# Performance work log

Measured on AMD Instinct MI355X. Metric: run time of the kernel, lower is better.

The kernel has to match this reference:

```python
import jax, jax.numpy as jnp
import numpy as np

ED = 1024
NH = 16
HD = ED // NH


def setup_inputs() -> dict:
    key = jax.random.key(0)
    ks = jax.random.split(key, 9)
    s = 1.0 / np.sqrt(ED)
    return {
        "x": jax.random.normal(ks[0], (2, 2048, ED), dtype=jnp.float32),
        "wq": jax.random.uniform(ks[1], (ED, ED), jnp.float32, -s, s),
        "bq": jax.random.uniform(ks[2], (ED,), jnp.float32, -s, s),
        "wk": jax.random.uniform(ks[3], (ED, ED), jnp.float32, -s, s),
        "bk": jax.random.uniform(ks[4], (ED,), jnp.float32, -s, s),
        "wv": jax.random.uniform(ks[5], (ED, ED), jnp.float32, -s, s),
        "bv": jax.random.uniform(ks[6], (ED,), jnp.float32, -s, s),
        "wo": jax.random.uniform(ks[7], (ED, ED), jnp.float32, -s, s),
        "bo": jax.random.uniform(ks[8], (ED,), jnp.float32, -s, s),
    }


def reference(x, wq, bq, wk, bk, wv, bv, wo, bo):
    B, N, _ = x.shape
    # projections; weights stored as [out, in] like nn.Linear -> x @ W.T + b
    def proj(w, b):
        y = jnp.einsum('bnd,ed->bne', x, w) + b
        return y.reshape(B, N, NH, HD).transpose(0, 2, 1, 3)  # [B, H, N, hd]
    Q, K, V = proj(wq, bq), proj(wk, bk), proj(wv, bv)
    scores = jnp.einsum('bhnd,bhmd->bhnm', Q, K) / jnp.sqrt(jnp.float32(HD))
    attn = jax.nn.softmax(scores, axis=-1)
    ctx = jnp.einsum('bhnm,bhmd->bhnd', attn, V)
    ctx = ctx.transpose(0, 2, 1, 3).reshape(B, N, ED)
    return jnp.einsum('bne,de->bnd', ctx, wo) + bo
```

## Files before the change

kernel.cpp:

```cpp
#include <hip/hip_runtime.h>
#include <hip/hip_bf16.h>

#define ED 1024
#define NH 16
#define HD 64
#define SEQ 2048

typedef float f32x4 __attribute__((ext_vector_type(4)));
typedef float f32x16 __attribute__((ext_vector_type(16)));
typedef short s16x8 __attribute__((ext_vector_type(8)));
typedef short s16x4 __attribute__((ext_vector_type(4)));
typedef __attribute__((address_space(1))) const unsigned int GBuf;
typedef __attribute__((address_space(3))) unsigned int LBuf;

#define QSC 0.18033688011112042f

union BF8 { s16x8 v; __hip_bfloat16 h[8]; };

__device__ __forceinline__ unsigned cvt_pk_bf16(float lo, float hi) {
  unsigned r;
  asm("v_cvt_pk_bf16_f32 %0, %1, %2" : "=v"(r) : "v"(lo), "v"(hi));
  return r;
}

__device__ __forceinline__ s16x8 pack_pfrag(float p0, float p1, float p2, float p3,
                                            float p4, float p5, float p6, float p7) {
  unsigned w0 = cvt_pk_bf16(p0, p1), w1 = cvt_pk_bf16(p2, p3);
  unsigned w2 = cvt_pk_bf16(p4, p5), w3 = cvt_pk_bf16(p6, p7);
  asm("v_permlane32_swap_b32 %0, %1" : "+v"(w0), "+v"(w2));
  asm("v_permlane32_swap_b32 %0, %1" : "+v"(w1), "+v"(w3));
  union { unsigned u[4]; s16x8 v; } r;
  r.u[0] = w0; r.u[1] = w1; r.u[2] = w2; r.u[3] = w3;
  return r.v;
}

__device__ inline void cvt_one(const float* __restrict__ s, __hip_bfloat16* __restrict__ d,
                               int n, int t, int stride) {
  const int n8 = n >> 3;
  for (int i = t; i < n8; i += stride) {
    const float4 u = ((const float4*)s)[2 * i];
    const float4 v = ((const float4*)s)[2 * i + 1];
    BF8 o;
    o.h[0] = __float2bfloat16(u.x); o.h[1] = __float2bfloat16(u.y);
    o.h[2] = __float2bfloat16(u.z); o.h[3] = __float2bfloat16(u.w);
    o.h[4] = __float2bfloat16(v.x); o.h[5] = __float2bfloat16(v.y);
    o.h[6] = __float2bfloat16(v.z); o.h[7] = __float2bfloat16(v.w);
    ((s16x8*)d)[i] = o.v;
  }
}

__global__ __launch_bounds__(256) void cvt5(const float* s0, const float* s1, const float* s2,
                                            const float* s3, const float* s4,
                                            __hip_bfloat16* d0, __hip_bfloat16* d1,
                                            __hip_bfloat16* d2, __hip_bfloat16* d3,
                                            __hip_bfloat16* d4,
                                            int n0, int n1, int n2, int n3, int n4) {
  const int stride = gridDim.x * blockDim.x;
  const int t = blockIdx.x * blockDim.x + threadIdx.x;
  cvt_one(s0, d0, n0, t, stride);
  cvt_one(s1, d1, n1, t, stride);
  cvt_one(s2, d2, n2, t, stride);
  cvt_one(s3, d3, n3, t, stride);
  cvt_one(s4, d4, n4, t, stride);
}

__global__ __launch_bounds__(256) void gemm_qkv(const __hip_bfloat16* __restrict__ A,
                                                const __hip_bfloat16* __restrict__ wq,
                                                const float* __restrict__ bq,
                                                const __hip_bfloat16* __restrict__ wk,
                                                const float* __restrict__ bk,
                                                const __hip_bfloat16* __restrict__ wv,
                                                const float* __restrict__ bv,
                                                __hip_bfloat16* __restrict__ Qo,
                                                __hip_bfloat16* __restrict__ Ko,
                                                __hip_bfloat16* __restrict__ Vo) {
  __shared__ __hip_bfloat16 As[2][128 * 64];
  __shared__ __hip_bfloat16 Bs[2][128 * 64];

  const int lin = (blockIdx.z * 32 + blockIdx.y) * 8 + blockIdx.x;
  const int work = (lin & 7) * 96 + (lin >> 3);
  const int z = work >> 8;
  const int rem = work & 255;
  const int m0 = (rem >> 3) * 128, n0 = (rem & 7) * 128;

  const __hip_bfloat16* W = (z == 0) ? wq : (z == 1) ? wk : wv;
  const float* bias = (z == 0) ? bq : (z == 1) ? bk : bv;

  const int tid = threadIdx.x;
  const int wave = tid >> 6, lane = tid & 63;
  const int ln15 = lane & 15, lg = lane >> 4;
  const int wr = (wave >> 1) * 64, wc = (wave & 1) * 64;

  f32x4 acc[4][4];
#pragma unroll
  for (int i = 0; i < 4; i++)
#pragma unroll
    for (int j = 0; j < 4; j++) acc[i][j] = (f32x4){0.f, 0.f, 0.f, 0.f};

  const int srow = tid >> 3;
  const int sk = (tid & 7) * 8;

  auto STAGE = [&](int t, int buf) {
    const int k0 = t * 64;
#pragma unroll
    for (int c = 0; c < 4; c++) {
      const int r = c * 32 + srow;
      __builtin_amdgcn_global_load_lds((GBuf*)(A + (size_t)(m0 + r) * ED + k0 + sk),
                                       (LBuf*)((char*)&As[buf][0] + c * 4096 + tid * 16), 16, 0, 0);
      __builtin_amdgcn_global_load_lds((GBuf*)(W + (size_t)(n0 + r) * ED + k0 + sk),
                                       (LBuf*)((char*)&Bs[buf][0] + c * 4096 + tid * 16), 16, 0, 0);
    }
  };

  const int NT = ED / 64;
  STAGE(0, 0);
  __syncthreads();
  for (int t = 0; t < NT; t++) {
    const int cur = t & 1;
    if (t + 1 < NT) STAGE(t + 1, cur ^ 1);
    __builtin_amdgcn_s_setprio(1);
#pragma unroll
    for (int kb = 0; kb < 2; kb++) {
      const int kof = kb * 32 + lg * 8;
      s16x8 a[4], b[4];
#pragma unroll
      for (int i = 0; i < 4; i++)
        a[i] = *(const s16x8*)&As[cur][(wr + i * 16 + ln15) * 64 + kof];
#pragma unroll
      for (int j = 0; j < 4; j++)
        b[j] = *(const s16x8*)&Bs[cur][(wc + j * 16 + ln15) * 64 + kof];
#pragma unroll
      for (int i = 0; i < 4; i++)
#pragma unroll
        for (int j = 0; j < 4; j++)
          acc[i][j] = __builtin_amdgcn_mfma_f32_16x16x32_bf16(a[i], b[j], acc[i][j], 0, 0, 0);
    }
    __builtin_amdgcn_s_setprio(0);
    __syncthreads();
  }

  const float scale = (z == 0) ? QSC : 1.0f;
  if (z < 2) {
    __hip_bfloat16* out = (z == 0) ? Qo : Ko;
#pragma unroll
    for (int j = 0; j < 4; j++) {
      const int e = n0 + wc + j * 16 + ln15;
      const float bvv = bias[e];
      const int h = e >> 6, hd = e & 63;
#pragma unroll
      for (int i = 0; i < 4; i++) {
#pragma unroll
        for (int r = 0; r < 4; r++) {
          const int m = m0 + wr + i * 16 + lg * 4 + r;
          const int b = m >> 11, n = m & 2047;
          out[(((size_t)(b * NH + h)) * SEQ + n) * HD + hd] =
              __float2bfloat16((acc[i][j][r] + bvv) * scale);
        }
      }
    }
  } else {
#pragma unroll
    for (int j = 0; j < 4; j++) {
      const int e = n0 + wc + j * 16 + ln15;
      const float bvv = bias[e];
      const int h = e >> 6, hd = e & 63;
#pragma unroll
      for (int i = 0; i < 4; i++) {
        const int m = m0 + wr + i * 16 + lg * 4;
        const int b = m >> 11, n = m & 2047;
        union { s16x4 v; __hip_bfloat16 hh[4]; } pk;
#pragma unroll
        for (int r = 0; r < 4; r++) pk.hh[r] = __float2bfloat16(acc[i][j][r] + bvv);
        *(s16x4*)&Vo[(((size_t)(b * NH + h)) * HD + hd) * SEQ + n] = pk.v;
      }
    }
  }
}

__global__ __launch_bounds__(256) void gemm_out(const __hip_bfloat16* __restrict__ A,
                                                const __hip_bfloat16* __restrict__ W,
                                                const float* __restrict__ bias,
                                                float* __restrict__ out) {
  __shared__ __hip_bfloat16 As[2][128 * 64];
  __shared__ __hip_bfloat16 Bs[2][128 * 64];

  const int lin = blockIdx.y * 8 + blockIdx.x;
  const int work = (lin & 7) * 32 + (lin >> 3);
  const int m0 = (work >> 3) * 128, n0 = (work & 7) * 128;

  const int tid = threadIdx.x;
  const int wave = tid >> 6, lane = tid & 63;
  const int ln15 = lane & 15, lg = lane >> 4;
  const int wr = (wave >> 1) * 64, wc = (wave & 1) * 64;

  f32x4 acc[4][4];
#pragma unroll
  for (int i = 0; i < 4; i++)
#pragma unroll
    for (int j = 0; j < 4; j++) acc[i][j] = (f32x4){0.f, 0.f, 0.f, 0.f};

  const int srow = tid >> 3;
  const int sk = (tid & 7) * 8;

  auto STAGE = [&](int t, int buf) {
    const int k0 = t * 64;
#pragma unroll
    for (int c = 0; c < 4; c++) {
      const int r = c * 32 + srow;
      __builtin_amdgcn_global_load_lds((GBuf*)(A + (size_t)(m0 + r) * ED + k0 + sk),
                                       (LBuf*)((char*)&As[buf][0] + c * 4096 + tid * 16), 16, 0, 0);
      __builtin_amdgcn_global_load_lds((GBuf*)(W + (size_t)(n0 + r) * ED + k0 + sk),
                                       (LBuf*)((char*)&Bs[buf][0] + c * 4096 + tid * 16), 16, 0, 0);
    }
  };

  const int NT = ED / 64;
  STAGE(0, 0);
  __syncthreads();
  for (int t = 0; t < NT; t++) {
    const int cur = t & 1;
    if (t + 1 < NT) STAGE(t + 1, cur ^ 1);
    __builtin_amdgcn_s_setprio(1);
#pragma unroll
    for (int kb = 0; kb < 2; kb++) {
      const int kof = kb * 32 + lg * 8;
      s16x8 a[4], b[4];
#pragma unroll
      for (int i = 0; i < 4; i++)
        a[i] = *(const s16x8*)&As[cur][(wr + i * 16 + ln15) * 64 + kof];
#pragma unroll
      for (int j = 0; j < 4; j++)
        b[j] = *(const s16x8*)&Bs[cur][(wc + j * 16 + ln15) * 64 + kof];
#pragma unroll
      for (int i = 0; i < 4; i++)
#pragma unroll
        for (int j = 0; j < 4; j++)
          acc[i][j] = __builtin_amdgcn_mfma_f32_16x16x32_bf16(a[i], b[j], acc[i][j], 0, 0, 0);
    }
    __builtin_amdgcn_s_setprio(0);
    __syncthreads();
  }

#pragma unroll
  for (int j = 0; j < 4; j++) {
    const int e = n0 + wc + j * 16 + ln15;
    const float bvv = bias[e];
#pragma unroll
    for (int i = 0; i < 4; i++)
#pragma unroll
      for (int r = 0; r < 4; r++) {
        const int m = m0 + wr + i * 16 + lg * 4 + r;
        out[(size_t)m * ED + e] = acc[i][j][r] + bvv;
      }
  }
}

__global__ __launch_bounds__(256) void attn_bf16(const __hip_bfloat16* __restrict__ Q,
                                                 const __hip_bfloat16* __restrict__ K,
                                                 const __hip_bfloat16* __restrict__ VT,
                                                 __hip_bfloat16* __restrict__ CTX) {
  __shared__ __hip_bfloat16 KsS[3][64 * 64];
  __shared__ __hip_bfloat16 VtS[3][64 * 64];

  const int tid = threadIdx.x;
  const int wave = tid >> 6, lane = tid & 63;
  const int l31 = lane & 31, hi = lane >> 5;
  const int rswz = l31 & 7;

  const int bid = blockIdx.x;
  const int work = (bid & 7) * 64 + (bid >> 3);
  const int qb = work & 15;
  const int bh = work >> 4;

  const __hip_bfloat16* Qh = Q + (size_t)bh * SEQ * HD;
  const __hip_bfloat16* Kh = K + (size_t)bh * SEQ * HD;
  const __hip_bfloat16* Vh = VT + (size_t)bh * HD * SEQ;

  const int q0 = qb * 128 + wave * 32;

  s16x8 aq[4];
#pragma unroll
  for (int kb = 0; kb < 4; kb++)
    aq[kb] = *(const s16x8*)&Qh[(size_t)(q0 + l31) * HD + kb * 16 + hi * 8];

  f32x16 acc0 = {}, acc1 = {};
  float m_ = -1e30f, l_ = 0.f;

  auto STAGE = [&](int kt_, int buf_) {
#pragma unroll
    for (int c = 0; c < 2; c++) {
      const int row = c * 32 + (tid >> 3);
      const int colb = ((tid & 7) * 16) ^ ((row & 7) << 4);
      __builtin_amdgcn_global_load_lds(
          (GBuf*)((const char*)Kh + ((size_t)(kt_ * 64 + row) * HD) * 2 + colb),
          (LBuf*)((char*)&KsS[buf_][0] + c * 4096 + tid * 16), 16, 0, 0);
      __builtin_amdgcn_global_load_lds(
          (GBuf*)((const char*)Vh + ((size_t)row * SEQ + kt_ * 64) * 2 + colb),
          (LBuf*)((char*)&VtS[buf_][0] + c * 4096 + tid * 16), 16, 0, 0);
    }
  };

  const int NT = SEQ / 64;
  STAGE(0, 0);
  STAGE(1, 1);

  for (int kt = 0; kt < NT; kt++) {
    const int cur = kt % 3;
    if (kt < NT - 1) {
      asm volatile("s_waitcnt vmcnt(4)" ::: "memory");
    } else {
      asm volatile("s_waitcnt vmcnt(0)" ::: "memory");
    }
    __builtin_amdgcn_sched_barrier(0);
    __builtin_amdgcn_s_barrier();
    if (kt + 2 < NT) STAGE(kt + 2, (kt + 2) % 3);

    f32x16 s0 = {}, s1 = {};
    __builtin_amdgcn_s_setprio(1);
#pragma unroll
    for (int kb = 0; kb < 4; kb++) {
      const int coff = ((kb * 2 + hi) ^ rswz) << 4;
      const s16x8 ak0 = *(const s16x8*)((const char*)&KsS[cur][0] + l31 * 128 + coff);
      const s16x8 ak1 = *(const s16x8*)((const char*)&KsS[cur][0] + (32 + l31) * 128 + coff);
      s0 = __builtin_amdgcn_mfma_f32_32x32x16_bf16(ak0, aq[kb], s0, 0, 0, 0);
      s1 = __builtin_amdgcn_mfma_f32_32x32x16_bf16(ak1, aq[kb], s1, 0, 0, 0);
    }
    __builtin_amdgcn_s_setprio(0);

    float t8[8];
#pragma unroll
    for (int i = 0; i < 8; i++)
      t8[i] = fmaxf(fmaxf(s0[i], s0[i + 8]), fmaxf(s1[i], s1[i + 8]));
    float tm = fmaxf(fmaxf(fmaxf(t8[0], t8[1]), fmaxf(t8[2], t8[3])),
                     fmaxf(fmaxf(t8[4], t8[5]), fmaxf(t8[6], t8[7])));
    tm = fmaxf(tm, __shfl_xor(tm, 32));

    if (!__all(tm - m_ <= 8.0f)) {
      const float mnew = fmaxf(m_, tm);
      const float fs = exp2f(m_ - mnew);
      m_ = mnew;
      l_ *= fs;
#pragma unroll
      for (int r = 0; r < 16; r++) { acc0[r] *= fs; acc1[r] *= fs; }
    }

#pragma unroll
    for (int r = 0; r < 16; r++) {
      s0[r] = exp2f(s0[r] - m_);
      s1[r] = exp2f(s1[r] - m_);
    }
    float sa[8];
#pragma unroll
    for (int i = 0; i < 8; i++) sa[i] = (s0[i] + s0[i + 8]) + (s1[i] + s1[i + 8]);
    float sum = ((sa[0] + sa[1]) + (sa[2] + sa[3])) + ((sa[4] + sa[5]) + (sa[6] + sa[7]));
    sum += __shfl_xor(sum, 32);
    l_ += sum;

    s16x8 pa[4];
    pa[0] = pack_pfrag(s0[0], s0[1], s0[2], s0[3], s0[4], s0[5], s0[6], s0[7]);
    pa[1] = pack_pfrag(s0[8], s0[9], s0[10], s0[11], s0[12], s0[13], s0[14], s0[15]);
    pa[2] = pack_pfrag(s1[0], s1[1], s1[2], s1[3], s1[4], s1[5], s1[6], s1[7]);
    pa[3] = pack_pfrag(s1[8], s1[9], s1[10], s1[11], s1[12], s1[13], s1[14], s1[15]);

    __builtin_amdgcn_s_setprio(1);
#pragma unroll
    for (int kp = 0; kp < 4; kp++) {
      const int coff = ((kp * 2 + hi) ^ rswz) << 4;
      const s16x8 av0 = *(const s16x8*)((const char*)&VtS[cur][0] + l31 * 128 + coff);
      const s16x8 av1 = *(const s16x8*)((const char*)&VtS[cur][0] + (32 + l31) * 128 + coff);
      acc0 = __builtin_amdgcn_mfma_f32_32x32x16_bf16(av0, pa[kp], acc0, 0, 0, 0);
      acc1 = __builtin_amdgcn_mfma_f32_32x32x16_bf16(av1, pa[kp], acc1, 0, 0, 0);
    }
    __builtin_amdgcn_s_setprio(0);
  }

  const float inv = 1.0f / l_;
  const int b = bh / NH, h = bh % NH;
  const int n = q0 + l31;
  __hip_bfloat16* dst = &CTX[((size_t)(b * SEQ + n)) * ED + h * HD];
#pragma unroll
  for (int g = 0; g < 4; g++) {
    union { s16x4 v; __hip_bfloat16 hh[4]; } p0, p1;
#pragma unroll
    for (int r = 0; r < 4; r++) {
      p0.hh[r] = __float2bfloat16(acc0[4 * g + r] * inv);
      p1.hh[r] = __float2bfloat16(acc1[4 * g + r] * inv);
    }
    *(s16x4*)&dst[8 * g + 4 * hi] = p0.v;
    *(s16x4*)&dst[32 + 8 * g + 4 * hi] = p1.v;
  }
}

extern "C" void kernel_launch(void* const* d_in, const int* in_sizes, int n_in,
                              void* d_out, int out_size, void* d_ws, size_t ws_size,
                              hipStream_t stream) {
  const float* x = (const float*)d_in[0];
  const float* wq = (const float*)d_in[1];
  const float* bq = (const float*)d_in[2];
  const float* wk = (const float*)d_in[3];
  const float* bk = (const float*)d_in[4];
  const float* wv = (const float*)d_in[5];
  const float* bv = (const float*)d_in[6];
  const float* wo = (const float*)d_in[7];
  const float* bo = (const float*)d_in[8];
  float* out = (float*)d_out;

  const int BN = in_sizes[0] / ED;

  char* w = (char*)d_ws;
  __hip_bfloat16* xbf = (__hip_bfloat16*)(w);
  __hip_bfloat16* wqb = (__hip_bfloat16*)(w + (8 << 20));
  __hip_bfloat16* wkb = (__hip_bfloat16*)(w + (10 << 20));
  __hip_bfloat16* wvb = (__hip_bfloat16*)(w + (12 << 20));
  __hip_bfloat16* wob = (__hip_bfloat16*)(w + (14 << 20));
  __hip_bfloat16* Qb = (__hip_bfloat16*)(w + (16 << 20));
  __hip_bfloat16* Kb = (__hip_bfloat16*)(w + (24 << 20));
  __hip_bfloat16* VTb = (__hip_bfloat16*)(w + (32 << 20));
  __hip_bfloat16* CTXb = (__hip_bfloat16*)(w + (40 << 20));

  cvt5<<<1024, 256, 0, stream>>>(x, wq, wk, wv, wo, xbf, wqb, wkb, wvb, wob,
                                 BN * ED, ED * ED, ED * ED, ED * ED, ED * ED);

  const dim3 blk(256);
  gemm_qkv<<<dim3(ED / 128, BN / 128, 3), blk, 0, stream>>>(
      xbf, wqb, bq, wkb, bk, wvb, bv, Qb, Kb, VTb);

  attn_bf16<<<dim3(512), blk, 0, stream>>>(Qb, Kb, VTb, CTXb);

  gemm_out<<<dim3(ED / 128, BN / 128), blk, 0, stream>>>(CTXb, wob, bo, out);
}
```

Baseline: 237.7 us.

## Split attention KV sequence across two wave groups and vectorize QK projection stores

The attention kernel now runs 512 threads per block. Two groups of four waves each handle alternating 64-key tiles of the same 128 queries, then merge their partial softmax states (max, sum, accumulator) through LDS at the end. This doubles the waves in flight for the 512-block grid, in exchange for a merge step, a lower register budget and a simpler double-buffered pipeline with full barriers. Separately, the Q/K projection swaps the MFMA operands so each lane holds four consecutive head-dim values, which allows packed 8-byte bf16 stores and float4 bias loads.

```diff
diff --git a/kernel.cpp b/kernel.cpp
--- a/kernel.cpp
+++ b/kernel.cpp
@@ -129,33 +129,42 @@
 #pragma unroll
       for (int j = 0; j < 4; j++)
         b[j] = *(const s16x8*)&Bs[cur][(wc + j * 16 + ln15) * 64 + kof];
-#pragma unroll
-      for (int i = 0; i < 4; i++)
-#pragma unroll
-        for (int j = 0; j < 4; j++)
-          acc[i][j] = __builtin_amdgcn_mfma_f32_16x16x32_bf16(a[i], b[j], acc[i][j], 0, 0, 0);
+      if (z < 2) {
+#pragma unroll
+        for (int i = 0; i < 4; i++)
+#pragma unroll
+          for (int j = 0; j < 4; j++)
+            acc[i][j] = __builtin_amdgcn_mfma_f32_16x16x32_bf16(b[j], a[i], acc[i][j], 0, 0, 0);
+      } else {
+#pragma unroll
+        for (int i = 0; i < 4; i++)
+#pragma unroll
+          for (int j = 0; j < 4; j++)
+            acc[i][j] = __builtin_amdgcn_mfma_f32_16x16x32_bf16(a[i], b[j], acc[i][j], 0, 0, 0);
+      }
     }
     __builtin_amdgcn_s_setprio(0);
     __syncthreads();
   }
 
-  const float scale = (z == 0) ? QSC : 1.0f;
   if (z < 2) {
+    const float scale = (z == 0) ? QSC : 1.0f;
     __hip_bfloat16* out = (z == 0) ? Qo : Ko;
 #pragma unroll
-    for (int j = 0; j < 4; j++) {
-      const int e = n0 + wc + j * 16 + ln15;
-      const float bvv = bias[e];
-      const int h = e >> 6, hd = e & 63;
-#pragma unroll
-      for (int i = 0; i < 4; i++) {
-#pragma unroll
-        for (int r = 0; r < 4; r++) {
-          const int m = m0 + wr + i * 16 + lg * 4 + r;
-          const int b = m >> 11, n = m & 2047;
-          out[(((size_t)(b * NH + h)) * SEQ + n) * HD + hd] =
-              __float2bfloat16((acc[i][j][r] + bvv) * scale);
-        }
+    for (int i = 0; i < 4; i++) {
+      const int m = m0 + wr + i * 16 + ln15;
+      const int b = m >> 11, n = m & 2047;
+#pragma unroll
+      for (int j = 0; j < 4; j++) {
+        const int e0 = n0 + wc + j * 16 + lg * 4;
+        const int h = e0 >> 6, hd = e0 & 63;
+        const float4 b4 = *(const float4*)&bias[e0];
+        union { s16x4 v; __hip_bfloat16 hh[4]; } pk;
+        pk.hh[0] = __float2bfloat16((acc[i][j][0] + b4.x) * scale);
+        pk.hh[1] = __float2bfloat16((acc[i][j][1] + b4.y) * scale);
+        pk.hh[2] = __float2bfloat16((acc[i][j][2] + b4.z) * scale);
+        pk.hh[3] = __float2bfloat16((acc[i][j][3] + b4.w) * scale);
+        *(s16x4*)&out[(((size_t)(b * NH + h)) * SEQ + n) * HD + hd] = pk.v;
       }
     }
   } else {
@@ -255,17 +264,20 @@
   }
 }
 
-__global__ __launch_bounds__(256) void attn_bf16(const __hip_bfloat16* __restrict__ Q,
-                                                 const __hip_bfloat16* __restrict__ K,
-                                                 const __hip_bfloat16* __restrict__ VT,
-                                                 __hip_bfloat16* __restrict__ CTX) {
-  __shared__ __hip_bfloat16 KsS[3][64 * 64];
-  __shared__ __hip_bfloat16 VtS[3][64 * 64];
+__global__ __launch_bounds__(512, 4) void attn_bf16(const __hip_bfloat16* __restrict__ Q,
+                                                    const __hip_bfloat16* __restrict__ K,
+                                                    const __hip_bfloat16* __restrict__ VT,
+                                                    __hip_bfloat16* __restrict__ CTX) {
+  __shared__ char ldsraw[65536];
+  float* mgacc = (float*)ldsraw;
+  float* mgml = (float*)(ldsraw + 4 * 32 * 66 * 4);
 
   const int tid = threadIdx.x;
   const int wave = tid >> 6, lane = tid & 63;
   const int l31 = lane & 31, hi = lane >> 5;
   const int rswz = l31 & 7;
+  const int par = wave >> 2;
+  const int wq = wave & 3;
 
   const int bid = blockIdx.x;
   const int work = (bid & 7) * 64 + (bid >> 3);
@@ -276,7 +288,7 @@
   const __hip_bfloat16* Kh = K + (size_t)bh * SEQ * HD;
   const __hip_bfloat16* Vh = VT + (size_t)bh * HD * SEQ;
 
-  const int q0 = qb * 128 + wave * 32;
+  const int q0 = qb * 128 + wq * 32;
 
   s16x8 aq[4];
 #pragma unroll
@@ -286,42 +298,40 @@
   f32x16 acc0 = {}, acc1 = {};
   float m_ = -1e30f, l_ = 0.f;
 
-  auto STAGE = [&](int kt_, int buf_) {
+  const int lt = tid & 255;
+  auto STAGE = [&](int tile, int buf) {
 #pragma unroll
     for (int c = 0; c < 2; c++) {
-      const int row = c * 32 + (tid >> 3);
-      const int colb = ((tid & 7) * 16) ^ ((row & 7) << 4);
+      const int row = c * 32 + (lt >> 3);
+      const int colb = ((lt & 7) * 16) ^ ((row & 7) << 4);
+      char* kbase = ldsraw + ((par * 2 + buf) * 2 + 0) * 8192;
+      char* vbase = ldsraw + ((par * 2 + buf) * 2 + 1) * 8192;
       __builtin_amdgcn_global_load_lds(
-          (GBuf*)((const char*)Kh + ((size_t)(kt_ * 64 + row) * HD) * 2 + colb),
-          (LBuf*)((char*)&KsS[buf_][0] + c * 4096 + tid * 16), 16, 0, 0);
+          (GBuf*)((const char*)Kh + ((size_t)(tile * 64 + row) * HD) * 2 + colb),
+          (LBuf*)(kbase + c * 4096 + lt * 16), 16, 0, 0);
       __builtin_amdgcn_global_load_lds(
-          (GBuf*)((const char*)Vh + ((size_t)row * SEQ + kt_ * 64) * 2 + colb),
-          (LBuf*)((char*)&VtS[buf_][0] + c * 4096 + tid * 16), 16, 0, 0);
+          (GBuf*)((const char*)Vh + ((size_t)row * SEQ + tile * 64) * 2 + colb),
+          (LBuf*)(vbase + c * 4096 + lt * 16), 16, 0, 0);
     }
   };
 
-  const int NT = SEQ / 64;
-  STAGE(0, 0);
-  STAGE(1, 1);
-
-  for (int kt = 0; kt < NT; kt++) {
-    const int cur = kt % 3;
-    if (kt < NT - 1) {
-      asm volatile("s_waitcnt vmcnt(4)" ::: "memory");
-    } else {
-      asm volatile("s_waitcnt vmcnt(0)" ::: "memory");
-    }
-    __builtin_amdgcn_sched_barrier(0);
-    __builtin_amdgcn_s_barrier();
-    if (kt + 2 < NT) STAGE(kt + 2, (kt + 2) % 3);
+  const int NI = SEQ / 128;
+  STAGE(par, 0);
+  for (int i = 0; i < NI; i++) {
+    const int cur = i & 1;
+    __syncthreads();
+    if (i + 1 < NI) STAGE(2 * (i + 1) + par, cur ^ 1);
+
+    const char* Ksb = ldsraw + ((par * 2 + cur) * 2 + 0) * 8192;
+    const char* Vtb = ldsraw + ((par * 2 + cur) * 2 + 1) * 8192;
 
     f32x16 s0 = {}, s1 = {};
     __builtin_amdgcn_s_setprio(1);
 #pragma unroll
     for (int kb = 0; kb < 4; kb++) {
       const int coff = ((kb * 2 + hi) ^ rswz) << 4;
-      const s16x8 ak0 = *(const s16x8*)((const char*)&KsS[cur][0] + l31 * 128 + coff);
-      const s16x8 ak1 = *(const s16x8*)((const char*)&KsS[cur][0] + (32 + l31) * 128 + coff);
+      const s16x8 ak0 = *(const s16x8*)(Ksb + l31 * 128 + coff);
+      const s16x8 ak1 = *(const s16x8*)(Ksb + (32 + l31) * 128 + coff);
       s0 = __builtin_amdgcn_mfma_f32_32x32x16_bf16(ak0, aq[kb], s0, 0, 0, 0);
       s1 = __builtin_amdgcn_mfma_f32_32x32x16_bf16(ak1, aq[kb], s1, 0, 0, 0);
     }
@@ -329,8 +339,8 @@
 
     float t8[8];
 #pragma unroll
-    for (int i = 0; i < 8; i++)
-      t8[i] = fmaxf(fmaxf(s0[i], s0[i + 8]), fmaxf(s1[i], s1[i + 8]));
+    for (int i2 = 0; i2 < 8; i2++)
+      t8[i2] = fmaxf(fmaxf(s0[i2], s0[i2 + 8]), fmaxf(s1[i2], s1[i2 + 8]));
     float tm = fmaxf(fmaxf(fmaxf(t8[0], t8[1]), fmaxf(t8[2], t8[3])),
                      fmaxf(fmaxf(t8[4], t8[5]), fmaxf(t8[6], t8[7])));
     tm = fmaxf(tm, __shfl_xor(tm, 32));
@@ -351,7 +361,7 @@
     }
     float sa[8];
 #pragma unroll
-    for (int i = 0; i < 8; i++) sa[i] = (s0[i] + s0[i + 8]) + (s1[i] + s1[i + 8]);
+    for (int i2 = 0; i2 < 8; i2++) sa[i2] = (s0[i2] + s0[i2 + 8]) + (s1[i2] + s1[i2 + 8]);
     float sum = ((sa[0] + sa[1]) + (sa[2] + sa[3])) + ((sa[4] + sa[5]) + (sa[6] + sa[7]));
     sum += __shfl_xor(sum, 32);
     l_ += sum;
@@ -366,28 +376,55 @@
 #pragma unroll
     for (int kp = 0; kp < 4; kp++) {
       const int coff = ((kp * 2 + hi) ^ rswz) << 4;
-      const s16x8 av0 = *(const s16x8*)((const char*)&VtS[cur][0] + l31 * 128 + coff);
-      const s16x8 av1 = *(const s16x8*)((const char*)&VtS[cur][0] + (32 + l31) * 128 + coff);
+      const s16x8 av0 = *(const s16x8*)(Vtb + l31 * 128 + coff);
+      const s16x8 av1 = *(const s16x8*)(Vtb + (32 + l31) * 128 + coff);
       acc0 = __builtin_amdgcn_mfma_f32_32x32x16_bf16(av0, pa[kp], acc0, 0, 0, 0);
       acc1 = __builtin_amdgcn_mfma_f32_32x32x16_bf16(av1, pa[kp], acc1, 0, 0, 0);
     }
     __builtin_amdgcn_s_setprio(0);
   }
 
-  const float inv = 1.0f / l_;
-  const int b = bh / NH, h = bh % NH;
-  const int n = q0 + l31;
-  __hip_bfloat16* dst = &CTX[((size_t)(b * SEQ + n)) * ED + h * HD];
-#pragma unroll
-  for (int g = 0; g < 4; g++) {
-    union { s16x4 v; __hip_bfloat16 hh[4]; } p0, p1;
-#pragma unroll
-    for (int r = 0; r < 4; r++) {
-      p0.hh[r] = __float2bfloat16(acc0[4 * g + r] * inv);
-      p1.hh[r] = __float2bfloat16(acc1[4 * g + r] * inv);
-    }
-    *(s16x4*)&dst[8 * g + 4 * hi] = p0.v;
-    *(s16x4*)&dst[32 + 8 * g + 4 * hi] = p1.v;
+  __syncthreads();
+  if (wave >= 4) {
+    const int w = wave - 4;
+    float* ap = &mgacc[(w * 32 + l31) * 66];
+#pragma unroll
+    for (int g = 0; g < 4; g++)
+#pragma unroll
+      for (int r = 0; r < 4; r++) {
+        ap[8 * g + 4 * hi + r] = acc0[4 * g + r];
+        ap[32 + 8 * g + 4 * hi + r] = acc1[4 * g + r];
+      }
+    if (hi == 0) {
+      mgml[(w * 2 + 0) * 32 + l31] = m_;
+      mgml[(w * 2 + 1) * 32 + l31] = l_;
+    }
+  }
+  __syncthreads();
+  if (wave < 4) {
+    const float m1 = mgml[(wave * 2 + 0) * 32 + l31];
+    const float l1 = mgml[(wave * 2 + 1) * 32 + l31];
+    const float mm = fmaxf(m_, m1);
+    const float f0 = exp2f(m_ - mm), f1 = exp2f(m1 - mm);
+    const float inv = 1.0f / (l_ * f0 + l1 * f1);
+    const float* ap = &mgacc[(wave * 32 + l31) * 66];
+
+    const int b = bh / NH, h = bh % NH;
+    const int n = q0 + l31;
+    __hip_bfloat16* dst = &CTX[((size_t)(b * SEQ + n)) * ED + h * HD];
+#pragma unroll
+    for (int g = 0; g < 4; g++) {
+      union { s16x4 v; __hip_bfloat16 hh[4]; } p0, p1;
+#pragma unroll
+      for (int r = 0; r < 4; r++) {
+        const float o0 = (acc0[4 * g + r] * f0 + ap[8 * g + 4 * hi + r] * f1) * inv;
+        const float o1 = (acc1[4 * g + r] * f0 + ap[32 + 8 * g + 4 * hi + r] * f1) * inv;
+        p0.hh[r] = __float2bfloat16(o0);
+        p1.hh[r] = __float2bfloat16(o1);
+      }
+      *(s16x4*)&dst[8 * g + 4 * hi] = p0.v;
+      *(s16x4*)&dst[32 + 8 * g + 4 * hi] = p1.v;
+    }
   }
 }
 
@@ -421,11 +458,10 @@
   cvt5<<<1024, 256, 0, stream>>>(x, wq, wk, wv, wo, xbf, wqb, wkb, wvb, wob,
                                  BN * ED, ED * ED, ED * ED, ED * ED, ED * ED);
 
-  const dim3 blk(256);
-  gemm_qkv<<<dim3(ED / 128, BN / 128, 3), blk, 0, stream>>>(
+  gemm_qkv<<<dim3(8, 32, 3), dim3(256), 0, stream>>>(
       xbf, wqb, bq, wkb, bk, wvb, bv, Qb, Kb, VTb);
 
-  attn_bf16<<<dim3(512), blk, 0, stream>>>(Qb, Kb, VTb, CTXb);
-
-  gemm_out<<<dim3(ED / 128, BN / 128), blk, 0, stream>>>(CTXb, wob, bo, out);
-}
+  attn_bf16<<<dim3(512), dim3(512), 0, stream>>>(Qb, Kb, VTb, CTXb);
+
+  gemm_out<<<dim3(8, 32), dim3(256), 0, stream>>>(CTXb, wob, bo, out);
+}
```

Result: faster. 219.2 us (-7.8%).
